# Optimization experiments

Hardware: AMD Instinct MI355X
Metric: run time of the kernel (lower is better)

Reference implementation:

```python
import jax, jax.numpy as jnp
import numpy as np

B, N, D_IN, D_OUT = 8, 2048, 256, 128
ROW_ZERO = 85 - 10  # hardcoded in original: a[:, 0:85-10] = 0 (zeros rows, dim 1)
NEG_BIG = -9.0e15
EPS = 1e-12  # F.normalize eps


def setup_inputs() -> dict:
    key = jax.random.key(0)
    k1, k2, k3, k4 = jax.random.split(key, 4)
    h = jax.random.normal(k1, (B, N, D_IN), dtype=jnp.float32)
    adj = jax.random.randint(k2, (B, N, N), 0, 2, dtype=jnp.int32)
    adj_eye = jax.random.randint(k3, (B, N, N), 0, 2, dtype=jnp.int32)
    # xavier_uniform with gain=1.414 for W [in, out]
    limit = 1.414 * np.sqrt(6.0 / (D_IN + D_OUT))
    W = jax.random.uniform(k4, (D_IN, D_OUT), minval=-limit, maxval=limit, dtype=jnp.float32)
    return {"h": h, "adj": adj, "adj_eye": adj_eye, "W": W}


def reference(h, adj, adj_eye, W):
    # Wh: [B, N, D_OUT]
    Wh = jnp.matmul(h, W)
    # L2-normalize along feature dim (F.normalize semantics: x / max(||x||, eps))
    norm = jnp.maximum(jnp.linalg.norm(Wh, axis=-1, keepdims=True), EPS)
    Whn = Wh / norm
    # dense cosine-similarity scores: [B, N, N]
    score = jnp.einsum("bnd,bmd->bnm", Whn, Whn)
    # double-sort top-k emulation (faithful to original, incl. row-wise zeroing bug)
    a_sorted = jnp.sort(score, axis=-1)
    idx1 = jnp.argsort(score, axis=-1)
    a_sorted = a_sorted.at[:, 0:ROW_ZERO, :].set(0.0)
    idx2 = jnp.argsort(idx1, axis=-1)  # inverse permutation
    attscore = jnp.take_along_axis(a_sorted, idx2, axis=-1)
    # adjacency mask + softmax over neighbors
    e = jnp.where(adj_eye > 0, attscore, NEG_BIG)
    attention = jax.nn.softmax(e, axis=-1)
    # (dropout is identity in eval mode)
    h_prime = jnp.matmul(attention, Wh)
    return jax.nn.elu(h_prime)
```

## Files before the change

### kernel.cpp

```cpp
#include <hip/hip_runtime.h>
#include <stdint.h>

#define NN   2048
#define DD   128
#define DIN  256
#define ROWZ 75

typedef float f32x4 __attribute__((ext_vector_type(4)));
typedef short bf16x8 __attribute__((ext_vector_type(8)));
typedef unsigned int u32x4 __attribute__((ext_vector_type(4)));
typedef unsigned int u32x2 __attribute__((ext_vector_type(2)));

__device__ __forceinline__ unsigned short f2bf(float x){
  union { float f; unsigned int u; } v; v.f = x;
  unsigned int u = v.u;
  u += 0x7fffu + ((u >> 16) & 1u);
  return (unsigned short)(u >> 16);
}
__device__ __forceinline__ float bf2f(unsigned short b){
  union { float f; unsigned int u; } v; v.u = ((unsigned int)b) << 16;
  return v.f;
}

__launch_bounds__(256, 2)
__global__ void wh_kernel(const float* __restrict__ h, const float* __restrict__ W,
                          unsigned short* __restrict__ whn, unsigned short* __restrict__ whT)
{
  __shared__ float hs[32][36];
  __shared__ float Ws[32][128];
  __shared__ float ssp[32][33];
  __shared__ float sinv[32];

  const int t  = threadIdx.x;
  const int r0 = blockIdx.x * 32;
  const int r4 = (t >> 5) * 4;
  const int d4 = (t & 31) * 4;

  float acc[4][4];
#pragma unroll
  for (int i = 0; i < 4; ++i)
#pragma unroll
    for (int j = 0; j < 4; ++j) acc[i][j] = 0.f;

  const int lrow = t >> 3;
  const int lkb  = (t & 7) * 4;

  for (int kt = 0; kt < 8; ++kt){
    __syncthreads();
    {
      const float* src = h + (size_t)(r0 + lrow) * DIN + kt * 32 + lkb;
      f32x4 a = *(const f32x4*)src;
#pragma unroll
      for (int e = 0; e < 4; ++e) hs[lkb + e][lrow] = a[e];
    }
    {
      const int k = t >> 3;
      const int d = (t & 7) * 16;
      const float* src = W + (size_t)(kt * 32 + k) * DD + d;
      float* dst = &Ws[k][d];
#pragma unroll
      for (int e = 0; e < 4; ++e) ((f32x4*)dst)[e] = ((const f32x4*)src)[e];
    }
    __syncthreads();
#pragma unroll
    for (int k = 0; k < 32; ++k){
      f32x4 w4 = *(const f32x4*)&Ws[k][d4];
      f32x4 ha = *(const f32x4*)&hs[k][r4];
#pragma unroll
      for (int i = 0; i < 4; ++i)
#pragma unroll
        for (int j = 0; j < 4; ++j)
          acc[i][j] += ha[i] * w4[j];
    }
  }

#pragma unroll
  for (int i = 0; i < 4; ++i){
    float s = acc[i][0]*acc[i][0] + acc[i][1]*acc[i][1]
            + acc[i][2]*acc[i][2] + acc[i][3]*acc[i][3];
    ssp[r4 + i][t & 31] = s;
  }
  __syncthreads();
  if (t < 32){
    float ss = 0.f;
#pragma unroll
    for (int c = 0; c < 32; ++c) ss += ssp[t][c];
    sinv[t] = 1.0f / fmaxf(sqrtf(ss), 1e-12f);
  }
  __syncthreads();

  const int bb = r0 >> 11;
  const int n0 = (r0 & 2047) + r4;

#pragma unroll
  for (int i = 0; i < 4; ++i){
    const float inv = sinv[r4 + i];
    unsigned int lo = (unsigned int)f2bf(acc[i][0]*inv) | ((unsigned int)f2bf(acc[i][1]*inv) << 16);
    unsigned int hi = (unsigned int)f2bf(acc[i][2]*inv) | ((unsigned int)f2bf(acc[i][3]*inv) << 16);
    u32x2 pk = { lo, hi };
    *(u32x2*)(whn + (size_t)(r0 + r4 + i) * DD + d4) = pk;
  }
#pragma unroll
  for (int j = 0; j < 4; ++j){
    u32x2 pk;
#pragma unroll
    for (int e = 0; e < 2; ++e)
      pk[e] = (unsigned int)f2bf(acc[2*e][j]) | ((unsigned int)f2bf(acc[2*e + 1][j]) << 16);
    *(u32x2*)(whT + ((size_t)(bb * DD + d4 + j)) * NN + n0) = pk;
  }
}

__launch_bounds__(256, 2)
__global__ void attn_kernel(const unsigned short* __restrict__ whn,
                            const unsigned short* __restrict__ whT,
                            const int* __restrict__ adj,
                            float* __restrict__ out)
{
  __shared__ unsigned short Vt[128 * 128];
  __shared__ unsigned short Pbuf[4][32 * 40];
  __shared__ float linv_s[32];

  const int t    = threadIdx.x;
  const int w    = t >> 6;
  const int l    = t & 63;
  const int quad = l >> 4;
  const int l16  = l & 15;
  const int b    = blockIdx.x >> 6;
  const int qbase = (blockIdx.x & 63) * 32;

  const unsigned short* whn_b = whn + (size_t)b * NN * DD;
  const unsigned short* whT_b = whT + (size_t)b * DD * NN;
  const int*            adj_b = adj + (size_t)b * NN * NN;

  bf16x8 qf[2][4];
#pragma unroll
  for (int s = 0; s < 2; ++s)
#pragma unroll
    for (int kc = 0; kc < 4; ++kc)
      qf[s][kc] = *(const bf16x8*)(whn_b + (size_t)(qbase + s*16 + l16) * DD + kc*32 + quad*8);

  f32x4 oacc[2][8];
  float lacc[2][4];
#pragma unroll
  for (int s = 0; s < 2; ++s){
#pragma unroll
    for (int dt = 0; dt < 8; ++dt) oacc[s][dt] = (f32x4){0.f, 0.f, 0.f, 0.f};
#pragma unroll
    for (int r = 0; r < 4; ++r) lacc[s][r] = 0.f;
  }

  unsigned short* const Pw = &Pbuf[w][0];

  int av[2][2][4];
#pragma unroll
  for (int f = 0; f < 2; ++f)
#pragma unroll
    for (int s = 0; s < 2; ++s)
#pragma unroll
      for (int r = 0; r < 4; ++r)
        av[f][s][r] = adj_b[(size_t)(qbase + s*16 + quad*4 + r) * NN + w*32 + f*16 + l16];

  for (int it = 0; it < 16; ++it){
    const int m0 = it * 128;
    __syncthreads();

#pragma unroll
    for (int ii = 0; ii < 8; ++ii){
      const int d   = w*32 + ii*4 + quad;
      const int gsw = l16 ^ (d & 7);
      const unsigned short* src = whT_b + (size_t)d * NN + m0 + gsw * 8;
      __builtin_amdgcn_global_load_lds(
          (const __attribute__((address_space(1))) void*)src,
          (__attribute__((address_space(3))) void*)&Vt[(w*32 + ii*4) * 128],
          16, 0, 0);
    }

    int av_n[2][2][4];
    {
      const int mnext = (it < 15) ? (m0 + 128) : 0;
#pragma unroll
      for (int f = 0; f < 2; ++f)
#pragma unroll
        for (int s = 0; s < 2; ++s)
#pragma unroll
          for (int r = 0; r < 4; ++r)
            av_n[f][s][r] = adj_b[(size_t)(qbase + s*16 + quad*4 + r) * NN + mnext + w*32 + f*16 + l16];
    }

    bf16x8 kf[2][4];
#pragma unroll
    for (int f = 0; f < 2; ++f)
#pragma unroll
      for (int kc = 0; kc < 4; ++kc)
        kf[f][kc] = *(const bf16x8*)(whn_b + (size_t)(m0 + w*32 + f*16 + l16) * DD + kc*32 + quad*8);

#pragma unroll
    for (int f = 0; f < 2; ++f){
#pragma unroll
      for (int s = 0; s < 2; ++s){
        f32x4 sc = (f32x4){0.f, 0.f, 0.f, 0.f};
#pragma unroll
        for (int kc = 0; kc < 4; ++kc)
          sc = __builtin_amdgcn_mfma_f32_16x16x32_bf16(qf[s][kc], kf[f][kc], sc, 0, 0, 0);
#pragma unroll
        for (int r = 0; r < 4; ++r){
          const int qrow = qbase + s*16 + quad*4 + r;
          float sv = (qrow < ROWZ) ? 0.f : sc[r];
          float p32 = (av[f][s][r] > 0) ? __expf(sv) : 0.f;
          unsigned short pb = f2bf(p32);
          lacc[s][r] += bf2f(pb);
          Pw[(s*16 + quad*4 + r) * 40 + f*16 + l16] = pb;
        }
      }
    }
    __syncthreads();

#pragma unroll
    for (int s = 0; s < 2; ++s){
      bf16x8 pfr = *(const bf16x8*)&Pw[(s*16 + l16) * 40 + quad*8];
#pragma unroll
      for (int dt = 0; dt < 8; ++dt){
        const int d  = dt*16 + l16;
        const int gg = (w*4 + quad) ^ (d & 7);
        bf16x8 vf = *(const bf16x8*)&Vt[d * 128 + gg * 8];
        oacc[s][dt] = __builtin_amdgcn_mfma_f32_16x16x32_bf16(pfr, vf, oacc[s][dt], 0, 0, 0);
      }
    }

#pragma unroll
    for (int f = 0; f < 2; ++f)
#pragma unroll
      for (int s = 0; s < 2; ++s)
#pragma unroll
        for (int r = 0; r < 4; ++r)
          av[f][s][r] = av_n[f][s][r];
  }

  {
    float* lredw = (float*)Pw;
#pragma unroll
    for (int s = 0; s < 2; ++s)
#pragma unroll
      for (int r = 0; r < 4; ++r)
        lredw[(s*16 + quad*4 + r) * 16 + l16] = lacc[s][r];
  }
  __syncthreads();
  if (t < 32){
    float sum = 0.f;
    for (int ww = 0; ww < 4; ++ww){
      const float* lr = (const float*)&Pbuf[ww][0];
#pragma unroll
      for (int c = 0; c < 16; ++c) sum += lr[t * 16 + c];
    }
    linv_s[t] = 1.0f / sum;
  }

  float* const ored = (float*)&Vt[0];
  for (int s = 0; s < 2; ++s){
    __syncthreads();
#pragma unroll
    for (int dt = 0; dt < 8; ++dt)
#pragma unroll
      for (int r = 0; r < 4; ++r)
        ored[w*2048 + (quad*4 + r)*128 + dt*16 + l16] = oacc[s][dt][r];
    __syncthreads();
#pragma unroll
    for (int j = 0; j < 8; ++j){
      const int o  = j*256 + t;
      const int ql = o >> 7, d = o & 127;
      float v = ored[ql*128 + d] + ored[2048 + ql*128 + d]
              + ored[4096 + ql*128 + d] + ored[6144 + ql*128 + d];
      v *= linv_s[s*16 + ql];
      v = (v > 0.f) ? v : expm1f(v);
      out[(size_t)(b*NN + qbase + s*16 + ql) * DD + d] = v;
    }
  }
}

extern "C" void kernel_launch(void* const* d_in, const int* in_sizes, int n_in,
                              void* d_out, int out_size, void* d_ws, size_t ws_size,
                              hipStream_t stream)
{
  const float* h       = (const float*)d_in[0];
  const int*   adj_eye = (const int*)d_in[2];
  const float* W       = (const float*)d_in[3];
  float*       out     = (float*)d_out;

  unsigned short* whn = (unsigned short*)d_ws;
  unsigned short* whT = whn + (size_t)16384 * 128;

  wh_kernel<<<512, 256, 0, stream>>>(h, W, whn, whT);
  attn_kernel<<<512, 256, 0, stream>>>(whn, whT, adj_eye, out);
}
```

Measured before the change: 300.3 us.

## Pack adjacency mask into bitmask in wh_kernel and consume bits in attention

The wh_kernel now also reads the int32 adjacency matrix and compresses it to a 1-bit-per-entry mask using wave ballots, writing it to workspace. The attention kernel stages each block's 32 mask rows (8 KB) into shared memory once and tests bits instead of streaming int32 adjacency values every iteration. Block-to-batch mapping is also interleaved so consecutive blocks hit different batches. The full 128 MB adjacency read still happens, but it moves into the first kernel where it can overlap with the matmul, and the attention kernel's memory traffic drops sharply. This costs extra register pressure and stores in wh_kernel.

```diff
diff --git a/kernel.cpp b/kernel.cpp
--- a/kernel.cpp
+++ b/kernel.cpp
@@ -10,6 +10,7 @@
 typedef short bf16x8 __attribute__((ext_vector_type(8)));
 typedef unsigned int u32x4 __attribute__((ext_vector_type(4)));
 typedef unsigned int u32x2 __attribute__((ext_vector_type(2)));
+typedef unsigned long long u64x2 __attribute__((ext_vector_type(2)));
 
 __device__ __forceinline__ unsigned short f2bf(float x){
   union { float f; unsigned int u; } v; v.f = x;
@@ -24,7 +25,9 @@
 
 __launch_bounds__(256, 2)
 __global__ void wh_kernel(const float* __restrict__ h, const float* __restrict__ W,
-                          unsigned short* __restrict__ whn, unsigned short* __restrict__ whT)
+                          const int* __restrict__ adje,
+                          unsigned short* __restrict__ whn, unsigned short* __restrict__ whT,
+                          unsigned long long* __restrict__ adjp)
 {
   __shared__ float hs[32][36];
   __shared__ float Ws[32][128];
@@ -36,6 +39,9 @@
   const int r4 = (t >> 5) * 4;
   const int d4 = (t & 31) * 4;
 
+  const int wv = t >> 6;
+  const int ln = t & 63;
+
   float acc[4][4];
 #pragma unroll
   for (int i = 0; i < 4; ++i)
@@ -62,6 +68,13 @@
       for (int e = 0; e < 4; ++e) ((f32x4*)dst)[e] = ((const f32x4*)src)[e];
     }
     __syncthreads();
+
+    const int grow = r0 + kt * 4 + wv;
+    const int* arow = adje + (size_t)grow * NN;
+    int pv[32];
+#pragma unroll
+    for (int j = 0; j < 32; ++j) pv[j] = arow[j * 64 + ln];
+
 #pragma unroll
     for (int k = 0; k < 32; ++k){
       f32x4 w4 = *(const f32x4*)&Ws[k][d4];
@@ -71,6 +84,16 @@
 #pragma unroll
         for (int j = 0; j < 4; ++j)
           acc[i][j] += ha[i] * w4[j];
+    }
+
+#pragma unroll
+    for (int j = 0; j < 32; j += 2){
+      unsigned long long mA = __ballot(pv[j] > 0);
+      unsigned long long mB = __ballot(pv[j + 1] > 0);
+      if (ln == 0){
+        u64x2 pk = { mA, mB };
+        *(u64x2*)(adjp + (size_t)grow * 32 + j) = pk;
+      }
     }
   }
 
@@ -113,24 +136,33 @@
 __launch_bounds__(256, 2)
 __global__ void attn_kernel(const unsigned short* __restrict__ whn,
                             const unsigned short* __restrict__ whT,
-                            const int* __restrict__ adj,
+                            const unsigned int* __restrict__ adjp,
                             float* __restrict__ out)
 {
   __shared__ unsigned short Vt[128 * 128];
   __shared__ unsigned short Pbuf[4][32 * 40];
   __shared__ float linv_s[32];
+  __shared__ unsigned int Ab[32 * 68];
 
   const int t    = threadIdx.x;
   const int w    = t >> 6;
   const int l    = t & 63;
   const int quad = l >> 4;
   const int l16  = l & 15;
-  const int b    = blockIdx.x >> 6;
-  const int qbase = (blockIdx.x & 63) * 32;
+  const int b     = blockIdx.x & 7;
+  const int qbase = (blockIdx.x >> 3) * 32;
 
   const unsigned short* whn_b = whn + (size_t)b * NN * DD;
   const unsigned short* whT_b = whT + (size_t)b * DD * NN;
-  const int*            adj_b = adj + (size_t)b * NN * NN;
+
+  {
+    const unsigned int* src = adjp + ((size_t)(b * NN + qbase + (t >> 3))) * 64 + (t & 7) * 8;
+    u32x4 a0 = *(const u32x4*)src;
+    u32x4 a1 = *(const u32x4*)(src + 4);
+    unsigned int* dst = &Ab[(t >> 3) * 68 + (t & 7) * 8];
+    *(u32x4*)dst = a0;
+    *(u32x4*)(dst + 4) = a1;
+  }
 
   bf16x8 qf[2][4];
 #pragma unroll
@@ -151,18 +183,16 @@
 
   unsigned short* const Pw = &Pbuf[w][0];
 
-  int av[2][2][4];
-#pragma unroll
-  for (int f = 0; f < 2; ++f)
-#pragma unroll
-    for (int s = 0; s < 2; ++s)
-#pragma unroll
-      for (int r = 0; r < 4; ++r)
-        av[f][s][r] = adj_b[(size_t)(qbase + s*16 + quad*4 + r) * NN + w*32 + f*16 + l16];
-
   for (int it = 0; it < 16; ++it){
     const int m0 = it * 128;
     __syncthreads();
+
+    bf16x8 kf[2][4];
+#pragma unroll
+    for (int f = 0; f < 2; ++f)
+#pragma unroll
+      for (int kc = 0; kc < 4; ++kc)
+        kf[f][kc] = *(const bf16x8*)(whn_b + (size_t)(m0 + w*32 + f*16 + l16) * DD + kc*32 + quad*8);
 
 #pragma unroll
     for (int ii = 0; ii < 8; ++ii){
@@ -175,24 +205,12 @@
           16, 0, 0);
     }
 
-    int av_n[2][2][4];
-    {
-      const int mnext = (it < 15) ? (m0 + 128) : 0;
-#pragma unroll
-      for (int f = 0; f < 2; ++f)
-#pragma unroll
-        for (int s = 0; s < 2; ++s)
-#pragma unroll
-          for (int r = 0; r < 4; ++r)
-            av_n[f][s][r] = adj_b[(size_t)(qbase + s*16 + quad*4 + r) * NN + mnext + w*32 + f*16 + l16];
-    }
-
-    bf16x8 kf[2][4];
-#pragma unroll
-    for (int f = 0; f < 2; ++f)
-#pragma unroll
-      for (int kc = 0; kc < 4; ++kc)
-        kf[f][kc] = *(const bf16x8*)(whn_b + (size_t)(m0 + w*32 + f*16 + l16) * DD + kc*32 + quad*8);
+    unsigned int aw[2][4];
+#pragma unroll
+    for (int s = 0; s < 2; ++s)
+#pragma unroll
+      for (int r = 0; r < 4; ++r)
+        aw[s][r] = Ab[(s*16 + quad*4 + r) * 68 + it*4 + w];
 
 #pragma unroll
     for (int f = 0; f < 2; ++f){
@@ -206,7 +224,7 @@
         for (int r = 0; r < 4; ++r){
           const int qrow = qbase + s*16 + quad*4 + r;
           float sv = (qrow < ROWZ) ? 0.f : sc[r];
-          float p32 = (av[f][s][r] > 0) ? __expf(sv) : 0.f;
+          float p32 = ((aw[s][r] >> (f*16 + l16)) & 1u) ? __expf(sv) : 0.f;
           unsigned short pb = f2bf(p32);
           lacc[s][r] += bf2f(pb);
           Pw[(s*16 + quad*4 + r) * 40 + f*16 + l16] = pb;
@@ -226,14 +244,6 @@
         oacc[s][dt] = __builtin_amdgcn_mfma_f32_16x16x32_bf16(pfr, vf, oacc[s][dt], 0, 0, 0);
       }
     }
-
-#pragma unroll
-    for (int f = 0; f < 2; ++f)
-#pragma unroll
-      for (int s = 0; s < 2; ++s)
-#pragma unroll
-        for (int r = 0; r < 4; ++r)
-          av[f][s][r] = av_n[f][s][r];
   }
 
   {
@@ -286,9 +296,10 @@
   const float* W       = (const float*)d_in[3];
   float*       out     = (float*)d_out;
 
-  unsigned short* whn = (unsigned short*)d_ws;
-  unsigned short* whT = whn + (size_t)16384 * 128;
-
-  wh_kernel<<<512, 256, 0, stream>>>(h, W, whn, whT);
-  attn_kernel<<<512, 256, 0, stream>>>(whn, whT, adj_eye, out);
-}
+  unsigned short* whn  = (unsigned short*)d_ws;
+  unsigned short* whT  = whn + (size_t)16384 * 128;
+  unsigned int*   adjp = (unsigned int*)(whT + (size_t)16384 * 128);
+
+  wh_kernel<<<512, 256, 0, stream>>>(h, W, adj_eye, whn, whT, (unsigned long long*)adjp);
+  attn_kernel<<<512, 256, 0, stream>>>(whn, whT, adjp, out);
+}
```

After: 490.3 us. 1.63x slower.
